# Kernel optimization log

Measured on AMD Instinct MI355X. Metric: run time of the kernel, lower is better.

## Reference

```python
import jax, jax.numpy as jnp
import numpy as np

EPS = 1e-5  # torch BatchNorm default


def setup_inputs() -> dict:
    key = jax.random.key(0)
    k1, k2, k3 = jax.random.split(key, 3)
    N, C, T, V, O = 64, 64, 300, 25, 64
    x = jax.random.normal(k1, (N, C, T, V), dtype=jnp.float32)
    # 24 = V-1 convs, each (O, C, 1, 2) -> packed as (V-1, O, C, 2), scaled like conv_init
    W = jax.random.normal(k2, (V - 1, O, C, 2), dtype=jnp.float32) * (1.0 / np.sqrt(2 * C))
    b = jax.random.normal(k3, (V - 1, O), dtype=jnp.float32) * 0.01
    gamma = jnp.ones((O,), dtype=jnp.float32)
    beta = jnp.zeros((O,), dtype=jnp.float32)
    return {"x": x, "W": W, "b": b, "gamma": gamma, "beta": beta}


def reference(x, W, b, gamma, beta):
    # x: (N, C, T, V); W: (V-1, O, C, 2); b: (V-1, O)
    # Math of the original loop: out[..., v] = sum_i W0_i @ x[..., v]
    #   + sum_i W1_i @ x[..., (v+i+1) % V] + sum_i b_i
    V = x.shape[-1]
    W0 = W[..., 0]  # (V-1, O, C)
    W1 = W[..., 1]  # (V-1, O, C)
    # identity-tap term: all W0 share the same column -> sum once
    S0 = W0.sum(axis=0)  # (O, C)
    out = jnp.einsum('oc,nctv->notv', S0, x)
    # circular term: source u = (v+i+1)%V  <=>  i = (u-v-1)%V, valid for u != v
    v_idx = jnp.arange(V)
    off = (v_idx[None, :] - v_idx[:, None] - 1) % V  # (V_target, V_source) -> i, equals V-1 when u==v
    W1p = jnp.concatenate([W1, jnp.zeros_like(W1[:1])], axis=0)  # index V-1 maps to zero (u==v excluded)
    Wg = W1p[off]  # (V, V, O, C), zero on the diagonal
    out = out + jnp.einsum('vuoc,nctu->notv', Wg, x)
    out = out + b.sum(axis=0)[None, :, None, None]
    # BatchNorm2d (training-mode batch stats, biased variance) + ReLU
    mean = out.mean(axis=(0, 2, 3), keepdims=True)
    var = out.var(axis=(0, 2, 3), keepdims=True)
    out = (out - mean) * jax.lax.rsqrt(var + EPS)
    out = out * gamma[None, :, None, None] + beta[None, :, None, None]
    return jax.nn.relu(out)
```

## Files before the change

### kernel.cpp

```cpp
#include <hip/hip_runtime.h>


typedef short  s16x8 __attribute__((ext_vector_type(8)));
typedef float  f32x4 __attribute__((ext_vector_type(4)));

#define NTHR_   256
#define RPB_    250
#define NBR_    30
#define TS_     260

__device__ __forceinline__ unsigned short f2bf(float f) {
  unsigned u = __builtin_bit_cast(unsigned, f);
  return (unsigned short)((u + 0x7FFFu + ((u >> 16) & 1u)) >> 16);
}

#define GLDS16(G, L)                                                           \
  __builtin_amdgcn_global_load_lds(                                            \
      (const __attribute__((address_space(1))) void*)(G),                      \
      (__attribute__((address_space(3))) void*)(L), 16, 0, 0);

__global__ void pack_w_kernel(const float* __restrict__ W, s16x8* __restrict__ Wg) {
  int idx = blockIdx.x * 256 + threadIdx.x;
  if (idx >= 12800) return;
  int lane  = idx & 63;
  int ni    = (idx >> 6) & 3;
  int chunk = (idx >> 8) & 1;
  int s     = idx >> 9;
  int o     = (ni << 4) + (lane & 15);
  int cbase = (chunk << 5) + ((lane >> 4) << 3);
  s16x8 h;
#pragma unroll
  for (int j = 0; j < 8; ++j) {
    int c = cbase + j;
    float val;
    if (s == 0) {
      val = 0.f;
      for (int i = 0; i < 24; ++i) val += W[((i * 64 + o) * 64 + c) * 2];
    } else {
      val = W[(((s - 1) * 64 + o) * 64 + c) * 2 + 1];
    }
    h[j] = (short)f2bf(val);
  }
  Wg[idx] = h;
}

#define ADV(J) { bool w_ = (u[J] == 24); u[J] = w_ ? 0 : u[J] + 1; \
                 aoc[J] += w_ ? -384 : 16; }
#define MM(RT, CT, AF, BF) \
  acc[RT][CT] = __builtin_amdgcn_mfma_f32_16x16x32_bf16(AF, BF, acc[RT][CT], 0, 0, 0);

#define SHIFT(S_, CUR, NXT, FUT)                                               \
  {                                                                            \
    int sq_ = (S_) + 2; sq_ = (sq_ > 24) ? 24 : sq_;                           \
    const char* g_ = (const char*)(Wg + sq_ * 512) + goff;                     \
    GLDS16(g_,        Bsh + (FUT) * 8192 + loff)                               \
    GLDS16(g_ + 1024, Bsh + (FUT) * 8192 + loff + 1024)                        \
    const char* bq_ = Bsh + (CUR) * 8192 + 4096 + (lane << 4);                 \
    __builtin_amdgcn_s_setprio(1);                                             \
    Aq0 = *(const s16x8*)(Ash + aoc[0] + 16384);                               \
    MM(0, 0, Ap0, Bp0) MM(0, 1, Ap0, Bp1)                                      \
    Bq0 = *(const s16x8*)(bq_);                                                \
    MM(0, 2, Ap0, Bp2) MM(0, 3, Ap0, Bp3)                                      \
    Aq1 = *(const s16x8*)(Ash + aoc[1] + 16384);                               \
    MM(1, 0, Ap1, Bp0) MM(1, 1, Ap1, Bp1)                                      \
    Bq1 = *(const s16x8*)(bq_ + 1024);                                         \
    MM(1, 2, Ap1, Bp2) MM(1, 3, Ap1, Bp3)                                      \
    Aq2 = *(const s16x8*)(Ash + aoc[2] + 16384);                               \
    MM(2, 0, Ap2, Bp0) MM(2, 1, Ap2, Bp1)                                      \
    Bq2 = *(const s16x8*)(bq_ + 2048);                                         \
    MM(2, 2, Ap2, Bp2) MM(2, 3, Ap2, Bp3)                                      \
    Aq3 = *(const s16x8*)(Ash + aoc[3] + 16384);                               \
    MM(3, 0, Ap3, Bp0) MM(3, 1, Ap3, Bp1)                                      \
    Bq3 = *(const s16x8*)(bq_ + 3072);                                         \
    MM(3, 2, Ap3, Bp2) MM(3, 3, Ap3, Bp3)                                      \
    __builtin_amdgcn_s_setprio(0);                                             \
    asm volatile("s_waitcnt vmcnt(2)" ::: "memory");                           \
    __builtin_amdgcn_s_barrier();                                              \
    __builtin_amdgcn_sched_barrier(0);                                         \
    const char* bp_ = Bsh + (NXT) * 8192 + (lane << 4);                        \
    __builtin_amdgcn_s_setprio(1);                                             \
    ADV(0) Ap0 = *(const s16x8*)(Ash + aoc[0]);                                \
    MM(0, 0, Aq0, Bq0) MM(0, 1, Aq0, Bq1)                                      \
    Bp0 = *(const s16x8*)(bp_);                                                \
    MM(0, 2, Aq0, Bq2) MM(0, 3, Aq0, Bq3)                                      \
    ADV(1) Ap1 = *(const s16x8*)(Ash + aoc[1]);                                \
    MM(1, 0, Aq1, Bq0) MM(1, 1, Aq1, Bq1)                                      \
    Bp1 = *(const s16x8*)(bp_ + 1024);                                         \
    MM(1, 2, Aq1, Bq2) MM(1, 3, Aq1, Bq3)                                      \
    ADV(2) Ap2 = *(const s16x8*)(Ash + aoc[2]);                                \
    MM(2, 0, Aq2, Bq0) MM(2, 1, Aq2, Bq1)                                      \
    Bp2 = *(const s16x8*)(bp_ + 2048);                                         \
    MM(2, 2, Aq2, Bq2) MM(2, 3, Aq2, Bq3)                                      \
    ADV(3) Ap3 = *(const s16x8*)(Ash + aoc[3]);                                \
    MM(3, 0, Aq3, Bq0) MM(3, 1, Aq3, Bq1)                                      \
    Bp3 = *(const s16x8*)(bp_ + 3072);                                         \
    MM(3, 2, Aq3, Bq2) MM(3, 3, Aq3, Bq3)                                      \
    __builtin_amdgcn_s_setprio(0);                                             \
  }

__global__ __launch_bounds__(NTHR_) void tap_mm_kernel(
    const float* __restrict__ x, const s16x8* __restrict__ Wg,
    float* __restrict__ out, float* __restrict__ partials) {
  __shared__ __align__(16) char Ash[32768];
  __shared__ __align__(16) char Bsh[24576];
  __shared__ float red2[512];
  int br = blockIdx.x, n = blockIdx.y;
  int r0 = br * RPB_;
  const float* xn = x + n * 480000 + r0;
  int tid = threadIdx.x;
  int wid = tid >> 6, lane = tid & 63;
  int l15 = lane & 15, lk = lane >> 4;
  int goff = (wid << 11) + (lane << 4);
  int loff = (wid << 11);

  {
    const char* g0 = (const char*)Wg + goff;
    GLDS16(g0,        Bsh + loff)
    GLDS16(g0 + 1024, Bsh + loff + 1024)
    const char* g1 = (const char*)(Wg + 512) + goff;
    GLDS16(g1,        Bsh + 8192 + loff)
    GLDS16(g1 + 1024, Bsh + 8192 + loff + 1024)
  }

#pragma unroll 2
  for (int it = 0; it < 8; ++it) {
    bool vld = tid < RPB_;
    s16x8 h;
#pragma unroll
    for (int j = 0; j < 8; ++j) {
      float f = vld ? xn[((it << 3) + j) * 7500 + tid] : 0.f;
      h[j] = (short)f2bf(f);
    }
    *(s16x8*)(Ash + (it << 12) + (tid << 4)) = h;
  }

  int u[4], aoc[4];
#pragma unroll
  for (int rt = 0; rt < 4; ++rt) {
    int srow = (wid << 6) + (rt << 4) + l15;
    u[rt]   = srow % 25;
    aoc[rt] = (lk << 12) + (srow << 4);
  }
  f32x4 acc[4][4];
#pragma unroll
  for (int rt = 0; rt < 4; ++rt)
#pragma unroll
    for (int ct = 0; ct < 4; ++ct) acc[rt][ct] = (f32x4){0.f, 0.f, 0.f, 0.f};

  __syncthreads();

  s16x8 Ap0 = *(const s16x8*)(Ash + aoc[0]);
  s16x8 Ap1 = *(const s16x8*)(Ash + aoc[1]);
  s16x8 Ap2 = *(const s16x8*)(Ash + aoc[2]);
  s16x8 Ap3 = *(const s16x8*)(Ash + aoc[3]);
  const char* b0_ = Bsh + (lane << 4);
  s16x8 Bp0 = *(const s16x8*)(b0_);
  s16x8 Bp1 = *(const s16x8*)(b0_ + 1024);
  s16x8 Bp2 = *(const s16x8*)(b0_ + 2048);
  s16x8 Bp3 = *(const s16x8*)(b0_ + 3072);
  s16x8 Aq0, Aq1, Aq2, Aq3, Bq0, Bq1, Bq2, Bq3;

  for (int base = 0; base < 24; base += 6) {
    SHIFT(base + 0, 0, 1, 2)
    SHIFT(base + 1, 1, 2, 0)
    SHIFT(base + 2, 2, 0, 1)
    SHIFT(base + 3, 0, 1, 2)
    SHIFT(base + 4, 1, 2, 0)
    SHIFT(base + 5, 2, 0, 1)
  }
  SHIFT(24, 0, 1, 2)

  float s1v[4] = {0.f, 0.f, 0.f, 0.f}, s2v[4] = {0.f, 0.f, 0.f, 0.f};
#pragma unroll
  for (int rt = 0; rt < 4; ++rt) {
#pragma unroll
    for (int qq = 0; qq < 4; ++qq) {
      int rloc = (wid << 6) + (rt << 4) + (lk << 2) + qq;
      if (rloc < RPB_) {
#pragma unroll
        for (int ct = 0; ct < 4; ++ct) {
          float val = acc[rt][ct][qq];
          s1v[ct] += val;
          s2v[ct] += val * val;
        }
      }
    }
  }
#pragma unroll
  for (int ct = 0; ct < 4; ++ct) {
    float a = s1v[ct], b = s2v[ct];
    a += __shfl_xor(a, 16); a += __shfl_xor(a, 32);
    b += __shfl_xor(b, 16); b += __shfl_xor(b, 32);
    if (lane < 16) {
      int base = ((((wid << 2) + ct) << 4) + l15) * 2;
      red2[base]     = a;
      red2[base + 1] = b;
    }
  }

  float* T = (float*)Ash;
  float* outb = out + n * 480000 + r0;
#pragma unroll
  for (int qt = 0; qt < 4; ++qt) {
    __syncthreads();
#pragma unroll
    for (int rt = 0; rt < 4; ++rt) {
      int row0 = (wid << 6) + (rt << 4) + (lk << 2);
      *(f32x4*)&T[l15 * TS_ + row0] = acc[rt][qt];
    }
    __syncthreads();
    if (qt == 0 && tid < 128) {
      int o = tid >> 1, m = tid & 1;
      int ct = o >> 4, ol = o & 15;
      float sres = 0.f;
#pragma unroll
      for (int w = 0; w < 4; ++w)
        sres += red2[((((w << 2) + ct) << 4) + ol) * 2 + m];
      int bl = n * NBR_ + br;
      partials[bl * 128 + m * 64 + o] = sres;
    }
#pragma unroll
    for (int it = 0; it < 8; ++it) {
      int idx = tid + it * NTHR_;
      if (idx < 2000) {
        int ol = idx / 125, r2 = idx - ol * 125;
        *(float2*)&outb[((qt << 4) + ol) * 7500 + (r2 << 1)] =
            *(float2*)&T[ol * TS_ + (r2 << 1)];
      }
    }
  }
}

__global__ void finalize_kernel(const float* __restrict__ part,
                                const float* __restrict__ gamma,
                                const float* __restrict__ beta,
                                float* __restrict__ scsh) {
  __shared__ float sm[512];
  int o = blockIdx.x;
  int tid = threadIdx.x;
  float s1 = 0.f, s2 = 0.f;
  for (int b = tid; b < 64 * NBR_; b += 256) {
    s1 += part[b * 128 + o];
    s2 += part[b * 128 + 64 + o];
  }
  sm[tid] = s1; sm[256 + tid] = s2;
  __syncthreads();
  for (int st = 128; st >= 1; st >>= 1) {
    if (tid < st) { sm[tid] += sm[tid + st]; sm[256 + tid] += sm[256 + tid + st]; }
    __syncthreads();
  }
  if (tid == 0) {
    const float inv = 1.0f / 480000.0f;
    float mean = sm[0] * inv;
    float var  = sm[256] * inv - mean * mean;
    float sc = gamma[o] * rsqrtf(var + 1e-5f);
    float sh = beta[o] - mean * sc;
    scsh[o]      = sc;
    scsh[64 + o] = sh;
  }
}

__global__ void bn_relu_kernel(float4* __restrict__ out, const float* __restrict__ scsh) {
  int i = blockIdx.x * blockDim.x + threadIdx.x;
  const int total = 7680000;
  int stride = gridDim.x * blockDim.x;
  for (; i < total; i += stride) {
    int o = (i / 1875) & 63;
    float sc = scsh[o], sh = scsh[64 + o];
    float4 v = out[i];
    v.x = fmaxf(fmaf(v.x, sc, sh), 0.f);
    v.y = fmaxf(fmaf(v.y, sc, sh), 0.f);
    v.z = fmaxf(fmaf(v.z, sc, sh), 0.f);
    v.w = fmaxf(fmaf(v.w, sc, sh), 0.f);
    out[i] = v;
  }
}

extern "C" void kernel_launch(void* const* d_in, const int* in_sizes, int n_in,
                              void* d_out, int out_size, void* d_ws, size_t ws_size,
                              hipStream_t stream) {
  const float* x     = (const float*)d_in[0];
  const float* W     = (const float*)d_in[1];
  const float* gamma = (const float*)d_in[3];
  const float* beta  = (const float*)d_in[4];
  float* out = (float*)d_out;

  char* ws = (char*)d_ws;
  s16x8* Wg       = (s16x8*)ws;
  float* partials = (float*)(ws + 204800);
  float* scsh     = (float*)(ws + 204800 + 983040);

  pack_w_kernel<<<dim3(50), dim3(256), 0, stream>>>(W, Wg);
  tap_mm_kernel<<<dim3(NBR_, 64), dim3(NTHR_), 0, stream>>>(x, Wg, out, partials);
  finalize_kernel<<<dim3(64), dim3(256), 0, stream>>>(partials, gamma, beta, scsh);
  bn_relu_kernel<<<dim3(2048), dim3(256), 0, stream>>>((float4*)out, scsh);
}
```

Baseline: 179.3 us.

## Stage weight taps in bulk LDS halves instead of a triple-buffered per-tap pipeline

Replaces the per-shift triple-buffered weight prefetch, which needed a barrier and waitcnt every tap, with two bulk loads of 13 and then 12 tap slices into about 138 KB of dynamic LDS. The MFMA loop then runs barrier-free over each half, with a single sync between the halves. This removes 25 per-step barriers and the setprio toggles. The cost is much larger LDS use, which drops occupancy to one block per CU, and an exposed load stall at the start and midpoint.

```diff
diff --git a/kernel.cpp b/kernel.cpp
--- a/kernel.cpp
+++ b/kernel.cpp
@@ -8,6 +8,7 @@
 #define RPB_    250
 #define NBR_    30
 #define TS_     260
+#define SMEMB_  141312
 
 __device__ __forceinline__ unsigned short f2bf(float f) {
   unsigned u = __builtin_bit_cast(unsigned, f);
@@ -49,14 +50,9 @@
 #define MM(RT, CT, AF, BF) \
   acc[RT][CT] = __builtin_amdgcn_mfma_f32_16x16x32_bf16(AF, BF, acc[RT][CT], 0, 0, 0);
 
-#define SHIFT(S_, CUR, NXT, FUT)                                               \
+#define PHA(CURB)                                                              \
   {                                                                            \
-    int sq_ = (S_) + 2; sq_ = (sq_ > 24) ? 24 : sq_;                           \
-    const char* g_ = (const char*)(Wg + sq_ * 512) + goff;                     \
-    GLDS16(g_,        Bsh + (FUT) * 8192 + loff)                               \
-    GLDS16(g_ + 1024, Bsh + (FUT) * 8192 + loff + 1024)                        \
-    const char* bq_ = Bsh + (CUR) * 8192 + 4096 + (lane << 4);                 \
-    __builtin_amdgcn_s_setprio(1);                                             \
+    const char* bq_ = Bsh + (CURB) + 4096 + (lane << 4);                       \
     Aq0 = *(const s16x8*)(Ash + aoc[0] + 16384);                               \
     MM(0, 0, Ap0, Bp0) MM(0, 1, Ap0, Bp1)                                      \
     Bq0 = *(const s16x8*)(bq_);                                                \
@@ -73,12 +69,11 @@
     MM(3, 0, Ap3, Bp0) MM(3, 1, Ap3, Bp1)                                      \
     Bq3 = *(const s16x8*)(bq_ + 3072);                                         \
     MM(3, 2, Ap3, Bp2) MM(3, 3, Ap3, Bp3)                                      \
-    __builtin_amdgcn_s_setprio(0);                                             \
-    asm volatile("s_waitcnt vmcnt(2)" ::: "memory");                           \
-    __builtin_amdgcn_s_barrier();                                              \
-    __builtin_amdgcn_sched_barrier(0);                                         \
-    const char* bp_ = Bsh + (NXT) * 8192 + (lane << 4);                        \
-    __builtin_amdgcn_s_setprio(1);                                             \
+  }
+
+#define PHB(NXTB)                                                              \
+  {                                                                            \
+    const char* bp_ = Bsh + (NXTB) + (lane << 4);                              \
     ADV(0) Ap0 = *(const s16x8*)(Ash + aoc[0]);                                \
     MM(0, 0, Aq0, Bq0) MM(0, 1, Aq0, Bq1)                                      \
     Bp0 = *(const s16x8*)(bp_);                                                \
@@ -95,15 +90,35 @@
     MM(3, 0, Aq3, Bq0) MM(3, 1, Aq3, Bq1)                                      \
     Bp3 = *(const s16x8*)(bp_ + 3072);                                         \
     MM(3, 2, Aq3, Bq2) MM(3, 3, Aq3, Bq3)                                      \
-    __builtin_amdgcn_s_setprio(0);                                             \
+  }
+
+#define PHB_NOB()                                                              \
+  {                                                                            \
+    ADV(0) Ap0 = *(const s16x8*)(Ash + aoc[0]);                                \
+    MM(0, 0, Aq0, Bq0) MM(0, 1, Aq0, Bq1) MM(0, 2, Aq0, Bq2) MM(0, 3, Aq0, Bq3)\
+    ADV(1) Ap1 = *(const s16x8*)(Ash + aoc[1]);                                \
+    MM(1, 0, Aq1, Bq0) MM(1, 1, Aq1, Bq1) MM(1, 2, Aq1, Bq2) MM(1, 3, Aq1, Bq3)\
+    ADV(2) Ap2 = *(const s16x8*)(Ash + aoc[2]);                                \
+    MM(2, 0, Aq2, Bq0) MM(2, 1, Aq2, Bq1) MM(2, 2, Aq2, Bq2) MM(2, 3, Aq2, Bq3)\
+    ADV(3) Ap3 = *(const s16x8*)(Ash + aoc[3]);                                \
+    MM(3, 0, Aq3, Bq0) MM(3, 1, Aq3, Bq1) MM(3, 2, Aq3, Bq2) MM(3, 3, Aq3, Bq3)\
+  }
+
+#define PHB_END()                                                              \
+  {                                                                            \
+    MM(0, 0, Aq0, Bq0) MM(0, 1, Aq0, Bq1) MM(0, 2, Aq0, Bq2) MM(0, 3, Aq0, Bq3)\
+    MM(1, 0, Aq1, Bq0) MM(1, 1, Aq1, Bq1) MM(1, 2, Aq1, Bq2) MM(1, 3, Aq1, Bq3)\
+    MM(2, 0, Aq2, Bq0) MM(2, 1, Aq2, Bq1) MM(2, 2, Aq2, Bq2) MM(2, 3, Aq2, Bq3)\
+    MM(3, 0, Aq3, Bq0) MM(3, 1, Aq3, Bq1) MM(3, 2, Aq3, Bq2) MM(3, 3, Aq3, Bq3)\
   }
 
 __global__ __launch_bounds__(NTHR_) void tap_mm_kernel(
     const float* __restrict__ x, const s16x8* __restrict__ Wg,
     float* __restrict__ out, float* __restrict__ partials) {
-  __shared__ __align__(16) char Ash[32768];
-  __shared__ __align__(16) char Bsh[24576];
-  __shared__ float red2[512];
+  extern __shared__ __align__(16) char smem[];
+  char* Ash  = smem;
+  char* Bsh  = smem + 32768;
+  float* red2 = (float*)(smem + 139264);
   int br = blockIdx.x, n = blockIdx.y;
   int r0 = br * RPB_;
   const float* xn = x + n * 480000 + r0;
@@ -113,13 +128,11 @@
   int goff = (wid << 11) + (lane << 4);
   int loff = (wid << 11);
 
-  {
-    const char* g0 = (const char*)Wg + goff;
-    GLDS16(g0,        Bsh + loff)
-    GLDS16(g0 + 1024, Bsh + loff + 1024)
-    const char* g1 = (const char*)(Wg + 512) + goff;
-    GLDS16(g1,        Bsh + 8192 + loff)
-    GLDS16(g1 + 1024, Bsh + 8192 + loff + 1024)
+#pragma unroll
+  for (int sl = 0; sl < 13; ++sl) {
+    const char* g = (const char*)Wg + sl * 8192 + goff;
+    GLDS16(g,        Bsh + sl * 8192 + loff)
+    GLDS16(g + 1024, Bsh + sl * 8192 + loff + 1024)
   }
 
 #pragma unroll 2
@@ -160,15 +173,37 @@
   s16x8 Bp3 = *(const s16x8*)(b0_ + 3072);
   s16x8 Aq0, Aq1, Aq2, Aq3, Bq0, Bq1, Bq2, Bq3;
 
-  for (int base = 0; base < 24; base += 6) {
-    SHIFT(base + 0, 0, 1, 2)
-    SHIFT(base + 1, 1, 2, 0)
-    SHIFT(base + 2, 2, 0, 1)
-    SHIFT(base + 3, 0, 1, 2)
-    SHIFT(base + 4, 1, 2, 0)
-    SHIFT(base + 5, 2, 0, 1)
-  }
-  SHIFT(24, 0, 1, 2)
+#pragma unroll
+  for (int s = 0; s < 12; ++s) {
+    PHA(s * 8192)
+    PHB((s + 1) * 8192)
+  }
+  PHA(12 * 8192)
+  PHB_NOB()
+
+  __builtin_amdgcn_s_barrier();
+  __builtin_amdgcn_sched_barrier(0);
+#pragma unroll
+  for (int sl = 0; sl < 12; ++sl) {
+    const char* g = (const char*)Wg + (13 + sl) * 8192 + goff;
+    GLDS16(g,        Bsh + sl * 8192 + loff)
+    GLDS16(g + 1024, Bsh + sl * 8192 + loff + 1024)
+  }
+  asm volatile("s_waitcnt vmcnt(0)" ::: "memory");
+  __builtin_amdgcn_s_barrier();
+  __builtin_amdgcn_sched_barrier(0);
+  Bp0 = *(const s16x8*)(b0_);
+  Bp1 = *(const s16x8*)(b0_ + 1024);
+  Bp2 = *(const s16x8*)(b0_ + 2048);
+  Bp3 = *(const s16x8*)(b0_ + 3072);
+
+#pragma unroll
+  for (int s = 0; s < 11; ++s) {
+    PHA(s * 8192)
+    PHB((s + 1) * 8192)
+  }
+  PHA(11 * 8192)
+  PHB_END()
 
   float s1v[4] = {0.f, 0.f, 0.f, 0.f}, s2v[4] = {0.f, 0.f, 0.f, 0.f};
 #pragma unroll
@@ -290,8 +325,11 @@
   float* partials = (float*)(ws + 204800);
   float* scsh     = (float*)(ws + 204800 + 983040);
 
+  (void)hipFuncSetAttribute((const void*)tap_mm_kernel,
+                            hipFuncAttributeMaxDynamicSharedMemorySize, SMEMB_);
+
   pack_w_kernel<<<dim3(50), dim3(256), 0, stream>>>(W, Wg);
-  tap_mm_kernel<<<dim3(NBR_, 64), dim3(NTHR_), 0, stream>>>(x, Wg, out, partials);
+  tap_mm_kernel<<<dim3(NBR_, 64), dim3(NTHR_), SMEMB_, stream>>>(x, Wg, out, partials);
   finalize_kernel<<<dim3(64), dim3(256), 0, stream>>>(partials, gamma, beta, scsh);
   bn_relu_kernel<<<dim3(2048), dim3(256), 0, stream>>>((float4*)out, scsh);
 }
```

Measured after the change: 221.3 us. 23.4% more time.
